# Optimization experiments

Hardware: AMD Instinct MI355X
Metric: run time of the kernel (lower is better)

## Reference

```python
import jax, jax.numpy as jnp
import numpy as np

NUM_HEADS = 8
WINDOW = 7      # window_size -> K = 49 neighbors
DILATION = 1


def setup_inputs() -> dict:
    key = jax.random.key(0)
    k1, k2, k3 = jax.random.split(key, 3)
    shape = (4, 256, 48, 48)  # [B, C, H, W], C = num_heads * d_head
    return {
        "q": jax.random.normal(k1, shape, jnp.float32),
        "k": jax.random.normal(k2, shape, jnp.float32),
        "v": jax.random.normal(k3, shape, jnp.float32),
    }


def _neighbors(x, window, dilation):
    # x: [B, h, d, H, W] -> [B, h, K, d, H, W] via pad-and-slice shifts
    B, h, d, H, W = x.shape
    r = window // 2
    p = r * dilation
    xp = jnp.pad(x, ((0, 0), (0, 0), (0, 0), (p, p), (p, p)))
    offs = [(i - r) * dilation for i in range(window)]
    sl = [xp[:, :, :, p + dy:p + dy + H, p + dx:p + dx + W]
          for dy in offs for dx in offs]
    return jnp.stack(sl, axis=2)


def _valid_mask(H, W, window, dilation):
    # [K, H, W] boolean: True where the shifted neighbor is in-bounds
    r = window // 2
    offs = np.array([(i - r) * dilation for i in range(window)])
    hy = np.arange(H)[None, :] + offs[:, None]  # [window, H]
    wx = np.arange(W)[None, :] + offs[:, None]  # [window, W]
    vh = (hy >= 0) & (hy < H)
    vw = (wx >= 0) & (wx < W)
    mask = vh[:, None, :, None] & vw[None, :, None, :]  # [window, window, H, W]
    return jnp.asarray(mask.reshape(window * window, H, W))


def reference(q, k, v):
    B, C, H, W = q.shape
    h = NUM_HEADS
    d = C // h
    qh = q.reshape(B, h, d, H, W)
    kh = k.reshape(B, h, d, H, W)
    vh = v.reshape(B, h, d, H, W)
    kn = _neighbors(kh, WINDOW, DILATION)  # [B,h,K,d,H,W]
    vn = _neighbors(vh, WINDOW, DILATION)
    mask = _valid_mask(H, W, WINDOW, DILATION)[None, None]  # [1,1,K,H,W]
    scores = jnp.einsum('bhdxy,bhkdxy->bhkxy', qh, kn) * (d ** -0.5)
    scores = jnp.where(mask, scores, jnp.finfo(scores.dtype).min)
    attn = jax.nn.softmax(scores, axis=2)
    out = jnp.einsum('bhkxy,bhkdxy->bhdxy', attn, vn)
    return out.reshape(B, C, H, W)  # merge_heads
```

## Files before the change

kernel.cpp:

```cpp
#include <hip/hip_runtime.h>


#define H_IMG 48
#define W_IMG 48
#define DHEAD 32
#define NH    8
#define RAD   3
#define TW    16
#define TH    6
#define NPART 4
#define CPL   8
#define HALO_W  (TW + 2*RAD)
#define HALO_H  (TH + 2*RAD)
#define HALO_PX (HALO_W * HALO_H)
#define CSTR    40
#define PLANE   (H_IMG * W_IMG)
#define NTHREADS (NPART * TW * TH)

__device__ __forceinline__ unsigned short f2b(float f) {
  union { float f; unsigned int u; } x; x.f = f;
  unsigned int r = x.u + 0x7FFFu + ((x.u >> 16) & 1u);
  return (unsigned short)(r >> 16);
}
__device__ __forceinline__ float lo_bf(unsigned int u) {
  union { unsigned int i; float f; } x; x.i = u << 16; return x.f;
}
__device__ __forceinline__ float hi_bf(unsigned int u) {
  union { unsigned int i; float f; } x; x.i = u & 0xffff0000u; return x.f;
}
__device__ __forceinline__ float dppadd1(float x) {
  int y = __builtin_amdgcn_update_dpp(0, __float_as_int(x), 0xB1, 0xF, 0xF, true);
  return x + __int_as_float(y);
}
__device__ __forceinline__ float dppadd2(float x) {
  int y = __builtin_amdgcn_update_dpp(0, __float_as_int(x), 0x4E, 0xF, 0xF, true);
  return x + __int_as_float(y);
}

__global__ __launch_bounds__(NTHREADS, 5)
void natten_f32_kernel(const float* __restrict__ q,
                       const float* __restrict__ k,
                       const float* __restrict__ v,
                       float* __restrict__ out) {
  __shared__ __align__(16) unsigned short kl[HALO_PX * CSTR];
  __shared__ __align__(16) unsigned short vl[HALO_PX * CSTR];

  const int part = threadIdx.x;
  const int qx   = threadIdx.y;
  const int qy   = threadIdx.z;
  const int tid  = part + NPART * qx + NPART * TW * qy;
  const int x0   = blockIdx.x * TW;
  const int y0   = blockIdx.y * TH;
  const size_t cbase = (size_t)blockIdx.z * DHEAD * PLANE;

  for (int i = tid; i < HALO_PX * 4; i += NTHREADS) {
    const int pix = i >> 2, chunk = i & 3;
    const int hy = pix / HALO_W;
    const int hx = pix - hy * HALO_W;
    const int gy = y0 - RAD + hy;
    const int gx = x0 - RAD + hx;
    unsigned int kp[4] = {0, 0, 0, 0}, vp[4] = {0, 0, 0, 0};
    if ((unsigned)gy < (unsigned)H_IMG && (unsigned)gx < (unsigned)W_IMG) {
      const size_t g = cbase + (size_t)(chunk * CPL) * PLANE + (size_t)gy * W_IMG + gx;
      const float* kb = k + g;
      const float* vb = v + g;
#pragma unroll
      for (int j = 0; j < 4; ++j) {
        kp[j] = (unsigned)f2b(kb[(2*j)*PLANE]) | ((unsigned)f2b(kb[(2*j+1)*PLANE]) << 16);
        vp[j] = (unsigned)f2b(vb[(2*j)*PLANE]) | ((unsigned)f2b(vb[(2*j+1)*PLANE]) << 16);
      }
    }
    uint4 kq = {kp[0], kp[1], kp[2], kp[3]};
    uint4 vq = {vp[0], vp[1], vp[2], vp[3]};
    *(uint4*)&kl[pix * CSTR + chunk * CPL] = kq;
    *(uint4*)&vl[pix * CSTR + chunk * CPL] = vq;
  }

  const int gqx = x0 + qx, gqy = y0 + qy;
  const float scale = 0.17677669529663687f;
  float qf[CPL];
#pragma unroll
  for (int j = 0; j < CPL; ++j)
    qf[j] = q[cbase + (size_t)(part * CPL + j) * PLANE + (size_t)gqy * W_IMG + gqx] * scale;

  __syncthreads();

  float den = 0.0f;
  float o[CPL];
#pragma unroll
  for (int j = 0; j < CPL; ++j) o[j] = 0.0f;

  for (int ry = 0; ry < 2 * RAD + 1; ++ry) {
    const int rowbase = (qy + ry) * HALO_W;
    const int gy = gqy + ry - RAD;
    const bool rowok = (unsigned)gy < (unsigned)H_IMG;
#pragma unroll
    for (int rx = 0; rx < 2 * RAD + 1; ++rx) {
      const int pix = rowbase + qx + rx;
      const uint4 kw = *(const uint4*)&kl[pix * CSTR + part * CPL];
      float acc;
      acc  = qf[0] * lo_bf(kw.x) + qf[1] * hi_bf(kw.x);
      acc += qf[2] * lo_bf(kw.y) + qf[3] * hi_bf(kw.y);
      acc += qf[4] * lo_bf(kw.z) + qf[5] * hi_bf(kw.z);
      acc += qf[6] * lo_bf(kw.w) + qf[7] * hi_bf(kw.w);
      acc = dppadd1(acc);
      acc = dppadd2(acc);

      const int gx = gqx + rx - RAD;
      const bool ok = rowok && ((unsigned)gx < (unsigned)W_IMG);
      const float pw = ok ? __expf(acc) : 0.0f;
      den += pw;

      const uint4 vw = *(const uint4*)&vl[pix * CSTR + part * CPL];
      o[0] += pw * lo_bf(vw.x);  o[1] += pw * hi_bf(vw.x);
      o[2] += pw * lo_bf(vw.y);  o[3] += pw * hi_bf(vw.y);
      o[4] += pw * lo_bf(vw.z);  o[5] += pw * hi_bf(vw.z);
      o[6] += pw * lo_bf(vw.w);  o[7] += pw * hi_bf(vw.w);
    }
  }

  const float rden = 1.0f / den;
#pragma unroll
  for (int j = 0; j < CPL; ++j)
    out[cbase + (size_t)(part * CPL + j) * PLANE + (size_t)gqy * W_IMG + gqx] = o[j] * rden;
}

extern "C" void kernel_launch(void* const* d_in, const int* in_sizes, int n_in,
                              void* d_out, int out_size, void* d_ws, size_t ws_size,
                              hipStream_t stream) {
  const float* q = (const float*)d_in[0];
  const float* k = (const float*)d_in[1];
  const float* v = (const float*)d_in[2];
  float* out = (float*)d_out;

  dim3 grid(W_IMG / TW, H_IMG / TH, 4 * NH);
  dim3 block(NPART, TW, TH);
  hipLaunchKernelGGL(natten_f32_kernel, grid, block, 0, stream, q, k, v, out);
}
```

Baseline: 102.9 us.

## Switch K/V/Q staging to fp16 and use fdot2 for neighbor scores

Stores K and V in shared memory as fp16 instead of bf16 and converts Q to packed fp16, so the QK dot products use the packed fdot2 instruction instead of unpacking bf16 to fp32 and doing scalar FMAs. The inner column loop is padded to 8 iterations, with an extra zeroed pixel at the end of the halo buffer, and boundary checks are precomputed into a column bitmask. The occupancy hint in launch bounds drops from 5 to 4. The trade-off is fp16 range and precision limits on the inputs, plus one wasted neighbor iteration per row.

```diff
diff --git a/kernel.cpp b/kernel.cpp
--- a/kernel.cpp
+++ b/kernel.cpp
@@ -17,17 +17,9 @@
 #define PLANE   (H_IMG * W_IMG)
 #define NTHREADS (NPART * TW * TH)
 
-__device__ __forceinline__ unsigned short f2b(float f) {
-  union { float f; unsigned int u; } x; x.f = f;
-  unsigned int r = x.u + 0x7FFFu + ((x.u >> 16) & 1u);
-  return (unsigned short)(r >> 16);
-}
-__device__ __forceinline__ float lo_bf(unsigned int u) {
-  union { unsigned int i; float f; } x; x.i = u << 16; return x.f;
-}
-__device__ __forceinline__ float hi_bf(unsigned int u) {
-  union { unsigned int i; float f; } x; x.i = u & 0xffff0000u; return x.f;
-}
+typedef _Float16 half_t;
+typedef half_t half2_t __attribute__((ext_vector_type(2)));
+
 __device__ __forceinline__ float dppadd1(float x) {
   int y = __builtin_amdgcn_update_dpp(0, __float_as_int(x), 0xB1, 0xF, 0xF, true);
   return x + __int_as_float(y);
@@ -37,13 +29,13 @@
   return x + __int_as_float(y);
 }
 
-__global__ __launch_bounds__(NTHREADS, 5)
+__global__ __launch_bounds__(NTHREADS, 4)
 void natten_f32_kernel(const float* __restrict__ q,
                        const float* __restrict__ k,
                        const float* __restrict__ v,
                        float* __restrict__ out) {
-  __shared__ __align__(16) unsigned short kl[HALO_PX * CSTR];
-  __shared__ __align__(16) unsigned short vl[HALO_PX * CSTR];
+  __shared__ __align__(16) unsigned short kl[(HALO_PX + 1) * CSTR];
+  __shared__ __align__(16) unsigned short vl[(HALO_PX + 1) * CSTR];
 
   const int part = threadIdx.x;
   const int qx   = threadIdx.y;
@@ -59,29 +51,46 @@
     const int hx = pix - hy * HALO_W;
     const int gy = y0 - RAD + hy;
     const int gx = x0 - RAD + hx;
-    unsigned int kp[4] = {0, 0, 0, 0}, vp[4] = {0, 0, 0, 0};
+    union { half2_t h2[4]; uint4 u; } kk, vv;
+    kk.u = make_uint4(0, 0, 0, 0);
+    vv.u = make_uint4(0, 0, 0, 0);
     if ((unsigned)gy < (unsigned)H_IMG && (unsigned)gx < (unsigned)W_IMG) {
       const size_t g = cbase + (size_t)(chunk * CPL) * PLANE + (size_t)gy * W_IMG + gx;
       const float* kb = k + g;
       const float* vb = v + g;
 #pragma unroll
       for (int j = 0; j < 4; ++j) {
-        kp[j] = (unsigned)f2b(kb[(2*j)*PLANE]) | ((unsigned)f2b(kb[(2*j+1)*PLANE]) << 16);
-        vp[j] = (unsigned)f2b(vb[(2*j)*PLANE]) | ((unsigned)f2b(vb[(2*j+1)*PLANE]) << 16);
+        half2_t a, b;
+        a.x = (half_t)kb[(2 * j) * PLANE];  a.y = (half_t)kb[(2 * j + 1) * PLANE];
+        b.x = (half_t)vb[(2 * j) * PLANE];  b.y = (half_t)vb[(2 * j + 1) * PLANE];
+        kk.h2[j] = a;  vv.h2[j] = b;
       }
     }
-    uint4 kq = {kp[0], kp[1], kp[2], kp[3]};
-    uint4 vq = {vp[0], vp[1], vp[2], vp[3]};
-    *(uint4*)&kl[pix * CSTR + chunk * CPL] = kq;
-    *(uint4*)&vl[pix * CSTR + chunk * CPL] = vq;
+    *(uint4*)&kl[pix * CSTR + chunk * CPL] = kk.u;
+    *(uint4*)&vl[pix * CSTR + chunk * CPL] = vv.u;
+  }
+  if (tid < 4) {
+    const uint4 z = make_uint4(0, 0, 0, 0);
+    *(uint4*)&kl[HALO_PX * CSTR + tid * CPL] = z;
+    *(uint4*)&vl[HALO_PX * CSTR + tid * CPL] = z;
   }
 
   const int gqx = x0 + qx, gqy = y0 + qy;
-  const float scale = 0.17677669529663687f;
-  float qf[CPL];
+  const float S = 0.17677669529663687f;
+  const size_t qoff = cbase + (size_t)gqy * W_IMG + gqx;
+  half2_t qp[4];
 #pragma unroll
-  for (int j = 0; j < CPL; ++j)
-    qf[j] = q[cbase + (size_t)(part * CPL + j) * PLANE + (size_t)gqy * W_IMG + gqx] * scale;
+  for (int j = 0; j < 4; ++j) {
+    qp[j].x = (half_t)(q[qoff + (size_t)(part * CPL + 2 * j) * PLANE] * S);
+    qp[j].y = (half_t)(q[qoff + (size_t)(part * CPL + 2 * j + 1) * PLANE] * S);
+  }
+
+  unsigned colmask = 0;
+#pragma unroll
+  for (int rx = 0; rx < 7; ++rx) {
+    const int gx = gqx + rx - RAD;
+    if ((unsigned)gx < (unsigned)W_IMG) colmask |= (1u << rx);
+  }
 
   __syncthreads();
 
@@ -91,38 +100,36 @@
   for (int j = 0; j < CPL; ++j) o[j] = 0.0f;
 
   for (int ry = 0; ry < 2 * RAD + 1; ++ry) {
-    const int rowbase = (qy + ry) * HALO_W;
     const int gy = gqy + ry - RAD;
-    const bool rowok = (unsigned)gy < (unsigned)H_IMG;
+    const unsigned mrow = ((unsigned)gy < (unsigned)H_IMG) ? colmask : 0u;
+    const int base = ((qy + ry) * HALO_W + qx) * CSTR + part * CPL;
+    const unsigned short* kb = &kl[base];
+    const unsigned short* vb = &vl[base];
 #pragma unroll
-    for (int rx = 0; rx < 2 * RAD + 1; ++rx) {
-      const int pix = rowbase + qx + rx;
-      const uint4 kw = *(const uint4*)&kl[pix * CSTR + part * CPL];
-      float acc;
-      acc  = qf[0] * lo_bf(kw.x) + qf[1] * hi_bf(kw.x);
-      acc += qf[2] * lo_bf(kw.y) + qf[3] * hi_bf(kw.y);
-      acc += qf[4] * lo_bf(kw.z) + qf[5] * hi_bf(kw.z);
-      acc += qf[6] * lo_bf(kw.w) + qf[7] * hi_bf(kw.w);
+    for (int rx = 0; rx < 8; ++rx) {
+      union { uint4 u; half2_t h[4]; } kw, vw;
+      kw.u = *(const uint4*)(kb + rx * CSTR);
+      vw.u = *(const uint4*)(vb + rx * CSTR);
+      float acc = __builtin_amdgcn_fdot2(qp[0], kw.h[0], 0.0f, false);
+      acc = __builtin_amdgcn_fdot2(qp[1], kw.h[1], acc, false);
+      acc = __builtin_amdgcn_fdot2(qp[2], kw.h[2], acc, false);
+      acc = __builtin_amdgcn_fdot2(qp[3], kw.h[3], acc, false);
       acc = dppadd1(acc);
       acc = dppadd2(acc);
-
-      const int gx = gqx + rx - RAD;
-      const bool ok = rowok && ((unsigned)gx < (unsigned)W_IMG);
-      const float pw = ok ? __expf(acc) : 0.0f;
-      den += pw;
-
-      const uint4 vw = *(const uint4*)&vl[pix * CSTR + part * CPL];
-      o[0] += pw * lo_bf(vw.x);  o[1] += pw * hi_bf(vw.x);
-      o[2] += pw * lo_bf(vw.y);  o[3] += pw * hi_bf(vw.y);
-      o[4] += pw * lo_bf(vw.z);  o[5] += pw * hi_bf(vw.z);
-      o[6] += pw * lo_bf(vw.w);  o[7] += pw * hi_bf(vw.w);
+      const float pe = __expf(acc);
+      const float p = (mrow & (1u << rx)) ? pe : 0.0f;
+      den += p;
+      o[0] += p * (float)vw.h[0].x;  o[1] += p * (float)vw.h[0].y;
+      o[2] += p * (float)vw.h[1].x;  o[3] += p * (float)vw.h[1].y;
+      o[4] += p * (float)vw.h[2].x;  o[5] += p * (float)vw.h[2].y;
+      o[6] += p * (float)vw.h[3].x;  o[7] += p * (float)vw.h[3].y;
     }
   }
 
   const float rden = 1.0f / den;
 #pragma unroll
   for (int j = 0; j < CPL; ++j)
-    out[cbase + (size_t)(part * CPL + j) * PLANE + (size_t)gqy * W_IMG + gqx] = o[j] * rden;
+    out[qoff + (size_t)(part * CPL + j) * PLANE] = o[j] * rden;
 }
 
 extern "C" void kernel_launch(void* const* d_in, const int* in_sizes, int n_in,
```

Result: no change. 102.3 us (-0.6%).
